# Performance work log

Measured on AMD Instinct MI355X. Metric: run time of the kernel, lower is better.

## Reference

```python
import jax, jax.numpy as jnp
import numpy as np
from jax import lax

STEP = 16
LEAK = 32
KSIZE = STEP + LEAK            # 48
PADDING = KSIZE + STEP         # 64
THETA = 20
FODEP = KSIZE                  # 48 (default fodep = response kernel size)
OUT_CH = 1
NEURONS = 64


def setup_inputs() -> dict:
    key = jax.random.key(0)
    k1, k2 = jax.random.split(key)
    # binary input spikes [batch, in_channel, synapses, time]
    input_spikes = jax.random.randint(k1, (128, 1, 256, 1000), 0, 2).astype(jnp.float32)
    # weight [out_channel*neurons, in_channel*synapses] in [0, 1) (post-STDP-like)
    weight = jax.random.uniform(k2, (64, 256), dtype=jnp.float32)
    return {"input_spikes": input_spikes, "weight": weight}


def _weight_kernel(weight):
    # StepFireLeak.get_weight_kernel: piecewise linear rise (1/step slope) then
    # leak decay, clipped at 0, time-flipped for causal convolution.
    t_axis = jnp.arange(KSIZE, dtype=weight.dtype)                 # [K]
    t_spike = t_axis / STEP                                        # [K]
    w = weight[..., None]                                          # [ON, CS, 1]
    t_leak = -(t_axis - w * STEP) / LEAK + w                       # [ON, CS, K]
    kernel = jnp.maximum(0.0, jnp.minimum(t_spike, t_leak))        # [ON, CS, K]
    return kernel[..., ::-1]


def _winner_takes_all(potentials):
    # potentials: [B, C, N, T] -> scan over time with carried depression state
    B, C, N, T = potentials.shape
    pot_t = jnp.transpose(potentials, (3, 0, 1, 2))                # [T, B, C, N]

    def step_fn(depression, p):
        # p: [B, C, N]; depression: [B, C] int32
        winner = jnp.argmax(p, axis=-1)                            # [B, C]
        maxval = jnp.max(p, axis=-1)                               # [B, C]
        spike = maxval > THETA
        cond = jnp.logical_and(spike, depression == 0)             # min_depression stays 0
        cond_i = cond.astype(jnp.int32)
        winners_t = jax.nn.one_hot(winner, N, dtype=jnp.int32) * cond_i[..., None]
        new_dep = jnp.maximum(0, depression + cond_i * (FODEP + 1) - 1)
        return new_dep, winners_t

    dep0 = jnp.zeros((B, C), dtype=jnp.int32)
    _, winners = lax.scan(step_fn, dep0, pot_t)                    # winners: [T, B, C, N]
    return jnp.transpose(winners, (1, 2, 3, 0))                    # [B, C, N, T]


def reference(input_spikes, weight):
    B, C, S, T = input_spikes.shape
    x = input_spikes.reshape(B, C * S, T)
    kernel = _weight_kernel(weight)                                # [ON, CS, K]
    pot = lax.conv_general_dilated(
        x, kernel, window_strides=(1,), padding=[(PADDING, PADDING)],
        dimension_numbers=("NCH", "OIH", "NCH"))                  # [B, ON, T+81]
    pot = pot.reshape(B, OUT_CH, NEURONS, -1) + (THETA // 2)
    return _winner_takes_all(pot)                                  # int32 spikes
```

## Files before the change

### kernel.cpp

```cpp
#include <hip/hip_runtime.h>

#define S_TOTAL   256
#define T_IN      1000
#define U_TOTAL   1081
#define NEUR      64
#define KJ        48
#define THETA_F   20.0f
#define HALF_TH   10.0f

#define U_SPAN    256
#define T_PAD     1328
#define B_ROWS    304
#define LDS_B     (B_ROWS * 256)
#define LDS_A     (2 * NEUR * 256)
#define A_JSTRIDE LDS_A

#define OUT_PER_B (NEUR * U_TOTAL)

typedef int v4i  __attribute__((ext_vector_type(4)));
typedef int v16i __attribute__((ext_vector_type(16)));

__device__ __forceinline__ void async16(const void* gsrc, void* ldsdst) {
    __builtin_amdgcn_global_load_lds(
        (const __attribute__((address_space(1))) unsigned int*)gsrc,
        (__attribute__((address_space(3))) unsigned int*)ldsdst, 16, 0, 0);
}

__global__ __launch_bounds__(256) void build_gtab_i8(const float* __restrict__ weight,
                                                     char* __restrict__ gtab) {
    int idx = blockIdx.x * 256 + threadIdx.x;
    if (idx >= KJ * 2 * NEUR * 256) return;
    int i  = idx & 15;
    int m  = (idx >> 4) & 15;
    int n  = (idx >> 8) & 63;
    int pl = (idx >> 14) & 1;
    int j  = idx >> 15;
    int s  = ((m ^ (n & 15)) << 4) | i;
    float w  = weight[n * S_TOTAL + s];
    float ts = (float)j * 0.0625f;
    float tl = -((float)j - w * 16.0f) * 0.03125f + w;
    float g  = fmaxf(0.0f, fminf(ts, tl));
    int fix = (int)rintf(g * 16384.0f);
    fix = min(fix, 16383);
    int d = pl ? (fix & 127) : (fix >> 7);
    gtab[idx] = (char)d;
}

__global__ __launch_bounds__(256) void build_xT(const float* __restrict__ x,
                                                char* __restrict__ xT) {
    __shared__ float Xl[64][257];
    const int tid = threadIdx.x;
    const int tp0 = blockIdx.x * 64;
    const int b   = blockIdx.y;
    const float* xb = x + (size_t)b * (S_TOTAL * T_IN);
    const int t0 = tp0 - 64;
    const int lane16 = tid & 15;
    const int srow   = tid >> 4;
    const int t = t0 + lane16 * 4;
    const bool in = (t >= 0) && (t + 3 < T_IN);
#pragma unroll
    for (int pass = 0; pass < 16; ++pass) {
        int s = pass * 16 + srow;
        float4 v = make_float4(0.f, 0.f, 0.f, 0.f);
        if (in) v = *(const float4*)(xb + s * T_IN + t);
        int k = lane16 * 4;
        Xl[k + 0][s] = v.x; Xl[k + 1][s] = v.y;
        Xl[k + 2][s] = v.z; Xl[k + 3][s] = v.w;
    }
    __syncthreads();
    for (int g2 = tid; g2 < 64 * 16; g2 += 256) {
        int tl = g2 >> 4, m = g2 & 15;
        int tp = tp0 + tl;
        if (tp >= T_PAD) continue;
        int q = m ^ (tp & 15);
        int wds[4];
#pragma unroll
        for (int wq = 0; wq < 4; ++wq) {
            int b0 = (Xl[tl][q * 16 + wq * 4 + 0] > 0.5f) ? 1 : 0;
            int b1 = (Xl[tl][q * 16 + wq * 4 + 1] > 0.5f) ? 1 : 0;
            int b2 = (Xl[tl][q * 16 + wq * 4 + 2] > 0.5f) ? 1 : 0;
            int b3 = (Xl[tl][q * 16 + wq * 4 + 3] > 0.5f) ? 1 : 0;
            wds[wq] = b0 | (b1 << 8) | (b2 << 16) | (b3 << 24);
        }
        v4i val = { wds[0], wds[1], wds[2], wds[3] };
        *(v4i*)(xT + ((size_t)b * T_PAD + tp) * 256 + m * 16) = val;
    }
}

__global__ __launch_bounds__(256, 1) void conv_i8(const char* __restrict__ xT,
                                                  const char* __restrict__ gtab,
                                                  float* __restrict__ maxv,
                                                  int*   __restrict__ argn) {
    __shared__ __align__(16) char lds[LDS_B + 2 * LDS_A];
    char* Bl = lds;

    const int tid  = threadIdx.x;
    const int wid  = tid >> 6;
    const int lane = tid & 63;
    const int col  = lane & 31;
    const int h    = lane >> 5;
    const int tile = blockIdx.x;
    const int b    = blockIdx.y;
    const int u0   = tile * U_SPAN;

    const char* xTb = xT + ((size_t)b * T_PAD + u0) * 256;
    for (int c = wid; c < LDS_B / 1024; c += 4)
        async16(xTb + c * 1024 + lane * 16, Bl + c * 1024);
    for (int c = wid; c < LDS_A / 1024; c += 4)
        async16(gtab + c * 1024 + lane * 16, lds + LDS_B + c * 1024);

    v16i acc[2][2][2];
    const v16i zc = {0,0,0,0,0,0,0,0,0,0,0,0,0,0,0,0};
#pragma unroll
    for (int sl = 0; sl < 2; ++sl)
#pragma unroll
        for (int nh = 0; nh < 2; ++nh)
#pragma unroll
            for (int pl = 0; pl < 2; ++pl) acc[sl][nh][pl] = zc;

    for (int j = 0; j < KJ; ++j) {
        __syncthreads();
        if (j < KJ - 1) {
            const char* gj = gtab + (size_t)(j + 1) * A_JSTRIDE;
            char* Ad = lds + LDS_B + ((j + 1) & 1) * LDS_A;
            for (int c = wid; c < LDS_A / 1024; c += 4)
                async16(gj + c * 1024 + lane * 16, Ad + c * 1024);
        }
        const char* Ab = lds + LDS_B + (j & 1) * LDS_A;
        const int ta = 32 * wid + col + 47 - j;
        const int tb = ta + 128;
#pragma unroll
        for (int c = 0; c < 8; ++c) {
            const int sb = c * 2 + h;
            v4i b0 = *(const v4i*)(Bl + ta * 256 + ((sb ^ (ta & 15)) << 4));
            v4i b1 = *(const v4i*)(Bl + tb * 256 + ((sb ^ (tb & 15)) << 4));
            const int aswz = (sb ^ (col & 15)) << 4;
#pragma unroll
            for (int pl = 0; pl < 2; ++pl) {
                v4i a0 = *(const v4i*)(Ab + (pl * 64 +      col) * 256 + aswz);
                v4i a1 = *(const v4i*)(Ab + (pl * 64 + 32 + col) * 256 + aswz);
                acc[0][0][pl] = __builtin_amdgcn_mfma_i32_32x32x32_i8(a0, b0, acc[0][0][pl], 0, 0, 0);
                acc[0][1][pl] = __builtin_amdgcn_mfma_i32_32x32x32_i8(a1, b0, acc[0][1][pl], 0, 0, 0);
                acc[1][0][pl] = __builtin_amdgcn_mfma_i32_32x32x32_i8(a0, b1, acc[1][0][pl], 0, 0, 0);
                acc[1][1][pl] = __builtin_amdgcn_mfma_i32_32x32x32_i8(a1, b1, acc[1][1][pl], 0, 0, 0);
            }
        }
    }

#pragma unroll
    for (int sl = 0; sl < 2; ++sl) {
        float best = -3.0e38f;
        int   bestn = 0;
#pragma unroll
        for (int nh = 0; nh < 2; ++nh)
#pragma unroll
            for (int r = 0; r < 16; ++r) {
                float v = (float)acc[sl][nh][0][r] * 0.0078125f
                        + (float)acc[sl][nh][1][r] * 6.103515625e-05f;
                int n = nh * 32 + (r & 3) + 8 * (r >> 2) + 4 * h;
                if (v > best || (v == best && n < bestn)) { best = v; bestn = n; }
            }
        float ov = __shfl_xor(best, 32);
        int   on = __shfl_xor(bestn, 32);
        if (ov > best || (ov == best && on < bestn)) { best = ov; bestn = on; }
        const int u = u0 + 32 * (wid + 4 * sl) + col;
        if (h == 0 && u < U_TOTAL) {
            maxv[b * U_TOTAL + u] = best + HALF_TH;
            argn[b * U_TOTAL + u] = bestn;
        }
    }
}

__global__ __launch_bounds__(256) void zero_out(int* __restrict__ out, int n4) {
    int4 z4 = make_int4(0, 0, 0, 0);
    int4* o4 = (int4*)out;
    int stride = gridDim.x * 256;
    for (int i = blockIdx.x * 256 + threadIdx.x; i < n4; i += stride) o4[i] = z4;
}

__global__ __launch_bounds__(64) void wta_kernel(const float* __restrict__ maxv,
                                                 const int*   __restrict__ argn,
                                                 int* __restrict__ out) {
    __shared__ float smv[U_TOTAL];
    __shared__ int   sarg[U_TOTAL];
    const int b   = blockIdx.x;
    const int tid = threadIdx.x;
    int* ob = out + (size_t)b * OUT_PER_B;

    for (int t = tid; t < U_TOTAL; t += 64) {
        smv[t]  = maxv[b * U_TOTAL + t];
        sarg[t] = argn[b * U_TOTAL + t];
    }
    __syncthreads();

    if (tid == 0) {
        int dep = 0;
        for (int t = 0; t < U_TOTAL; ++t) {
            if (dep == 0) {
                if (smv[t] > THETA_F) {
                    ob[sarg[t] * U_TOTAL + t] = 1;
                    dep = 48;
                }
            } else {
                dep = dep - 1;
            }
        }
    }
}

extern "C" void kernel_launch(void* const* d_in, const int* in_sizes, int n_in,
                              void* d_out, int out_size, void* d_ws, size_t ws_size,
                              hipStream_t stream) {
    const float* x      = (const float*)d_in[0];
    const float* weight = (const float*)d_in[1];
    int* out = (int*)d_out;

    char*  ws   = (char*)d_ws;
    char*  xT   = ws;
    char*  gtab = ws + (size_t)128 * T_PAD * 256;
    float* maxv = (float*)(gtab + (size_t)KJ * 2 * NEUR * 256);
    int*   argn = (int*)((char*)maxv + (size_t)128 * U_TOTAL * 4);

    hipLaunchKernelGGL(build_gtab_i8, dim3((KJ * 2 * NEUR * 256) / 256), dim3(256),
                       0, stream, weight, gtab);
    hipLaunchKernelGGL(build_xT, dim3((T_PAD + 63) / 64, 128), dim3(256),
                       0, stream, x, xT);
    hipLaunchKernelGGL(zero_out, dim3(2048), dim3(256),
                       0, stream, out, (128 * OUT_PER_B) / 4);
    hipLaunchKernelGGL(conv_i8, dim3((U_TOTAL + U_SPAN - 1) / U_SPAN, 128), dim3(256),
                       0, stream, xT, gtab, maxv, argn);
    hipLaunchKernelGGL(wta_kernel, dim3(128), dim3(64),
                       0, stream, maxv, argn, out);
}
```

Before: 487.5 us.

## Bit-pack input spikes and expand in registers; parallelize WTA scan with ballot

The transposed input is stored as packed bits (40 bytes per time row) instead of one int8 per synapse, and conv_i8 expands the 16-bit groups to int8 vectors with a multiply-and-mask trick before each MFMA. This cuts xT write and read traffic and shrinks the LDS B buffer, which lets launch bounds allow two blocks per CU. The WTA pass now uses a wave ballot over 64 time steps and skips ahead by the refractory period instead of a serial per-step loop. The cost is extra ALU work in the MFMA inner loop to unpack the bits.

```diff
diff --git a/kernel.cpp b/kernel.cpp
--- a/kernel.cpp
+++ b/kernel.cpp
@@ -10,8 +10,8 @@
 
 #define U_SPAN    256
 #define T_PAD     1328
-#define B_ROWS    304
-#define LDS_B     (B_ROWS * 256)
+#define XROW      40
+#define LDS_BB    12288
 #define LDS_A     (2 * NEUR * 256)
 #define A_JSTRIDE LDS_A
 
@@ -24,6 +24,15 @@
     __builtin_amdgcn_global_load_lds(
         (const __attribute__((address_space(1))) unsigned int*)gsrc,
         (__attribute__((address_space(3))) unsigned int*)ldsdst, 16, 0, 0);
+}
+
+__device__ __forceinline__ v4i expand16(unsigned int n16) {
+    v4i r;
+    r[0] = (int)((((n16      ) & 15u) * 0x00204081u) & 0x01010101u);
+    r[1] = (int)((((n16 >> 4 ) & 15u) * 0x00204081u) & 0x01010101u);
+    r[2] = (int)((((n16 >> 8 ) & 15u) * 0x00204081u) & 0x01010101u);
+    r[3] = (int)((((n16 >> 12) & 15u) * 0x00204081u) & 0x01010101u);
+    return r;
 }
 
 __global__ __launch_bounds__(256) void build_gtab_i8(const float* __restrict__ weight,
@@ -48,50 +57,56 @@
 
 __global__ __launch_bounds__(256) void build_xT(const float* __restrict__ x,
                                                 char* __restrict__ xT) {
-    __shared__ float Xl[64][257];
+    __shared__ float Xl[32][324];
     const int tid = threadIdx.x;
-    const int tp0 = blockIdx.x * 64;
+    const int tp0 = blockIdx.x * 32;
     const int b   = blockIdx.y;
     const float* xb = x + (size_t)b * (S_TOTAL * T_IN);
     const int t0 = tp0 - 64;
-    const int lane16 = tid & 15;
-    const int srow   = tid >> 4;
-    const int t = t0 + lane16 * 4;
+    const int lane8 = tid & 7;
+    const int srow  = tid >> 3;
+    const int t = t0 + lane8 * 4;
     const bool in = (t >= 0) && (t + 3 < T_IN);
 #pragma unroll
-    for (int pass = 0; pass < 16; ++pass) {
-        int s = pass * 16 + srow;
+    for (int pass = 0; pass < 8; ++pass) {
+        int s = pass * 32 + srow;
         float4 v = make_float4(0.f, 0.f, 0.f, 0.f);
         if (in) v = *(const float4*)(xb + s * T_IN + t);
-        int k = lane16 * 4;
-        Xl[k + 0][s] = v.x; Xl[k + 1][s] = v.y;
-        Xl[k + 2][s] = v.z; Xl[k + 3][s] = v.w;
+        int colv = 20 * (s >> 4) + (s & 15);
+        int k = lane8 * 4;
+        Xl[k + 0][colv] = v.x; Xl[k + 1][colv] = v.y;
+        Xl[k + 2][colv] = v.z; Xl[k + 3][colv] = v.w;
     }
     __syncthreads();
-    for (int g2 = tid; g2 < 64 * 16; g2 += 256) {
-        int tl = g2 >> 4, m = g2 & 15;
-        int tp = tp0 + tl;
-        if (tp >= T_PAD) continue;
-        int q = m ^ (tp & 15);
-        int wds[4];
-#pragma unroll
-        for (int wq = 0; wq < 4; ++wq) {
-            int b0 = (Xl[tl][q * 16 + wq * 4 + 0] > 0.5f) ? 1 : 0;
-            int b1 = (Xl[tl][q * 16 + wq * 4 + 1] > 0.5f) ? 1 : 0;
-            int b2 = (Xl[tl][q * 16 + wq * 4 + 2] > 0.5f) ? 1 : 0;
-            int b3 = (Xl[tl][q * 16 + wq * 4 + 3] > 0.5f) ? 1 : 0;
-            wds[wq] = b0 | (b1 << 8) | (b2 << 16) | (b3 << 24);
-        }
-        v4i val = { wds[0], wds[1], wds[2], wds[3] };
-        *(v4i*)(xT + ((size_t)b * T_PAD + tp) * 256 + m * 16) = val;
-    }
-}
-
-__global__ __launch_bounds__(256, 1) void conv_i8(const char* __restrict__ xT,
+    {
+        const int tl = tid >> 3;
+        const int dw = tid & 7;
+        const int tp = tp0 + tl;
+        if (tp < T_PAD) {
+            unsigned bits = 0u;
+#pragma unroll
+            for (int gg = 0; gg < 2; ++gg) {
+                int g = 2 * dw + gg;
+#pragma unroll
+                for (int q = 0; q < 4; ++q) {
+                    float4 f = *(const float4*)&Xl[tl][20 * g + 4 * q];
+                    int z = gg * 16 + 4 * q;
+                    bits |= (f.x > 0.5f ? 1u : 0u) << (z + 0);
+                    bits |= (f.y > 0.5f ? 1u : 0u) << (z + 1);
+                    bits |= (f.z > 0.5f ? 1u : 0u) << (z + 2);
+                    bits |= (f.w > 0.5f ? 1u : 0u) << (z + 3);
+                }
+            }
+            *(unsigned*)(xT + ((size_t)b * T_PAD + tp) * XROW + 4 * dw) = bits;
+        }
+    }
+}
+
+__global__ __launch_bounds__(256, 2) void conv_i8(const char* __restrict__ xT,
                                                   const char* __restrict__ gtab,
                                                   float* __restrict__ maxv,
                                                   int*   __restrict__ argn) {
-    __shared__ __align__(16) char lds[LDS_B + 2 * LDS_A];
+    __shared__ __align__(16) char lds[LDS_BB + 2 * LDS_A];
     char* Bl = lds;
 
     const int tid  = threadIdx.x;
@@ -103,11 +118,11 @@
     const int b    = blockIdx.y;
     const int u0   = tile * U_SPAN;
 
-    const char* xTb = xT + ((size_t)b * T_PAD + u0) * 256;
-    for (int c = wid; c < LDS_B / 1024; c += 4)
+    const char* xTb = xT + ((size_t)b * T_PAD + u0) * XROW;
+    for (int c = wid; c < LDS_BB / 1024; c += 4)
         async16(xTb + c * 1024 + lane * 16, Bl + c * 1024);
     for (int c = wid; c < LDS_A / 1024; c += 4)
-        async16(gtab + c * 1024 + lane * 16, lds + LDS_B + c * 1024);
+        async16(gtab + c * 1024 + lane * 16, lds + LDS_BB + c * 1024);
 
     v16i acc[2][2][2];
     const v16i zc = {0,0,0,0,0,0,0,0,0,0,0,0,0,0,0,0};
@@ -122,18 +137,20 @@
         __syncthreads();
         if (j < KJ - 1) {
             const char* gj = gtab + (size_t)(j + 1) * A_JSTRIDE;
-            char* Ad = lds + LDS_B + ((j + 1) & 1) * LDS_A;
+            char* Ad = lds + LDS_BB + ((j + 1) & 1) * LDS_A;
             for (int c = wid; c < LDS_A / 1024; c += 4)
                 async16(gj + c * 1024 + lane * 16, Ad + c * 1024);
         }
-        const char* Ab = lds + LDS_B + (j & 1) * LDS_A;
+        const char* Ab = lds + LDS_BB + (j & 1) * LDS_A;
         const int ta = 32 * wid + col + 47 - j;
         const int tb = ta + 128;
 #pragma unroll
         for (int c = 0; c < 8; ++c) {
             const int sb = c * 2 + h;
-            v4i b0 = *(const v4i*)(Bl + ta * 256 + ((sb ^ (ta & 15)) << 4));
-            v4i b1 = *(const v4i*)(Bl + tb * 256 + ((sb ^ (tb & 15)) << 4));
+            unsigned ba = *(const unsigned short*)(Bl + ta * XROW + sb * 2);
+            unsigned bb = *(const unsigned short*)(Bl + tb * XROW + sb * 2);
+            v4i b0 = expand16(ba);
+            v4i b1 = expand16(bb);
             const int aswz = (sb ^ (col & 15)) << 4;
 #pragma unroll
             for (int pl = 0; pl < 2; ++pl) {
@@ -181,28 +198,32 @@
 __global__ __launch_bounds__(64) void wta_kernel(const float* __restrict__ maxv,
                                                  const int*   __restrict__ argn,
                                                  int* __restrict__ out) {
-    __shared__ float smv[U_TOTAL];
-    __shared__ int   sarg[U_TOTAL];
+    __shared__ int sarg[U_TOTAL];
     const int b   = blockIdx.x;
     const int tid = threadIdx.x;
     int* ob = out + (size_t)b * OUT_PER_B;
 
-    for (int t = tid; t < U_TOTAL; t += 64) {
-        smv[t]  = maxv[b * U_TOTAL + t];
+    for (int t = tid; t < U_TOTAL; t += 64)
         sarg[t] = argn[b * U_TOTAL + t];
-    }
     __syncthreads();
 
-    if (tid == 0) {
-        int dep = 0;
-        for (int t = 0; t < U_TOTAL; ++t) {
-            if (dep == 0) {
-                if (smv[t] > THETA_F) {
-                    ob[sarg[t] * U_TOTAL + t] = 1;
-                    dep = 48;
-                }
-            } else {
-                dep = dep - 1;
+    int cur = 0;
+#pragma unroll
+    for (int c = 0; c < 17; ++c) {
+        int t = c * 64 + tid;
+        float mv = (t < U_TOTAL) ? maxv[b * U_TOTAL + t] : -1.0f;
+        unsigned long long mask = __ballot(mv > THETA_F);
+        if (tid == 0 && mask) {
+            int base = c * 64;
+            while (true) {
+                int lo = cur - base;
+                if (lo >= 64) break;
+                if (lo < 0) lo = 0;
+                unsigned long long m = mask >> lo;
+                if (!m) break;
+                int ts = base + lo + __builtin_ctzll(m);
+                ob[sarg[ts] * U_TOTAL + ts] = 1;
+                cur = ts + 49;
             }
         }
     }
@@ -217,13 +238,13 @@
 
     char*  ws   = (char*)d_ws;
     char*  xT   = ws;
-    char*  gtab = ws + (size_t)128 * T_PAD * 256;
+    char*  gtab = ws + ((size_t)128 * T_PAD * XROW + 2048);
     float* maxv = (float*)(gtab + (size_t)KJ * 2 * NEUR * 256);
     int*   argn = (int*)((char*)maxv + (size_t)128 * U_TOTAL * 4);
 
     hipLaunchKernelGGL(build_gtab_i8, dim3((KJ * 2 * NEUR * 256) / 256), dim3(256),
                        0, stream, weight, gtab);
-    hipLaunchKernelGGL(build_xT, dim3((T_PAD + 63) / 64, 128), dim3(256),
+    hipLaunchKernelGGL(build_xT, dim3((T_PAD + 31) / 32, 128), dim3(256),
                        0, stream, x, xT);
     hipLaunchKernelGGL(zero_out, dim3(2048), dim3(256),
                        0, stream, out, (128 * OUT_PER_B) / 4);
```

After: 404.5 us. 1.21x faster.
